# Performance work log

Hardware: AMD Instinct MI355X
Metric: run time of the kernel (lower is better)

The kernel has to match this reference:

```python
import jax, jax.numpy as jnp
import numpy as np

NUM_HEADS = 16

def setup_inputs() -> dict:
    key = jax.random.key(0)
    ks = jax.random.split(key, 8)
    B, S, D = 2, 2048, 1024
    w = lambda k: jax.random.normal(k, (D, D), dtype=jnp.float32) * 0.02
    return {
        "x": jax.random.normal(ks[0], (B, S, D), dtype=jnp.float32),
        "attn_mask": jnp.zeros((S, S), dtype=jnp.float32),
        "key_padding_mask": jnp.zeros((B, S), dtype=bool),
        "Wq": w(ks[1]), "bq": jnp.zeros((D,), jnp.float32),
        "Wk": w(ks[2]), "bk": jnp.zeros((D,), jnp.float32),
        "Wv": w(ks[3]), "bv": jnp.zeros((D,), jnp.float32),
        "Wg": w(ks[4]), "bg": jnp.full((D,), 0.5, jnp.float32),  # gate_bias_init=0.5
        "Wo": w(ks[5]), "bo": jnp.zeros((D,), jnp.float32),
    }

def reference(x, attn_mask, key_padding_mask, Wq, bq, Wk, bk, Wv, bv, Wg, bg, Wo, bo):
    B, S, D = x.shape
    H = NUM_HEADS
    hd = D // H
    scale = jnp.sqrt(jnp.float32(hd)).astype(x.dtype)

    def split_heads(t):  # (B,S,D) -> (B,H,S,hd)
        return t.reshape(B, S, H, hd).transpose(0, 2, 1, 3)

    q = split_heads(x @ Wq + bq)
    k = split_heads(x @ Wk + bk)
    v = split_heads(x @ Wv + bv)

    scores = jnp.einsum("bhqd,bhkd->bhqk", q, k) / scale
    scores = scores + attn_mask[None, None, :, :]
    scores = jnp.where(key_padding_mask[:, None, None, :], -jnp.inf, scores)

    attn_weights = jax.nn.softmax(scores, axis=-1)          # (B,H,S,S)
    attn_out = jnp.einsum("bhqk,bhkd->bhqd", attn_weights, v)

    gate = jax.nn.sigmoid(x @ Wg + bg)                      # (B,S,D)
    gate = split_heads(gate)                                # (B,H,S,hd)
    attn_out = attn_out * gate

    attn_out = attn_out.transpose(0, 2, 1, 3).reshape(B, S, D)
    output = attn_out @ Wo + bo
    avg_attn = attn_weights.mean(axis=1)                    # (B,S,S)
    return output, avg_attn
```

## Files before the change

kernel.cpp:

```cpp
#include <hip/hip_runtime.h>
#include <hip/hip_bf16.h>

#define LOG2E 1.4426950408889634f

typedef short short8 __attribute__((ext_vector_type(8)));
typedef float floatx4 __attribute__((ext_vector_type(4)));

__device__ __forceinline__ floatx4 mfma16(short8 a, short8 b, floatx4 c) {
    return __builtin_amdgcn_mfma_f32_16x16x32_bf16(a, b, c, 0, 0, 0);
}

__device__ __forceinline__ float fexp2(float x) { return __builtin_amdgcn_exp2f(x); }

__device__ __forceinline__ short f2bf(float f) {
    unsigned u = __builtin_bit_cast(unsigned, f);
    u += 0x7FFFu + ((u >> 16) & 1u);
    return (short)(u >> 16);
}
__device__ __forceinline__ unsigned bfpair(float a, float b) {
    unsigned ua = __builtin_bit_cast(unsigned, a);
    unsigned ub = __builtin_bit_cast(unsigned, b);
    ua += 0x7FFFu + ((ua >> 16) & 1u);
    ub += 0x7FFFu + ((ub >> 16) & 1u);
    return (ua >> 16) | (ub & 0xFFFF0000u);
}
__device__ __forceinline__ float bf2f(short s) {
    unsigned u = ((unsigned)(unsigned short)s) << 16;
    return __builtin_bit_cast(float, u);
}

__device__ __forceinline__ void glds16(const void* g, void* l) {
    __builtin_amdgcn_global_load_lds(
        (const __attribute__((address_space(1))) void*)g,
        (__attribute__((address_space(3))) void*)l, 16, 0, 0);
}

__device__ __forceinline__ short8 cvt8(const float* __restrict__ p) {
    float4 a = *reinterpret_cast<const float4*>(p);
    float4 b = *reinterpret_cast<const float4*>(p + 4);
    short8 r;
    r[0] = f2bf(a.x); r[1] = f2bf(a.y); r[2] = f2bf(a.z); r[3] = f2bf(a.w);
    r[4] = f2bf(b.x); r[5] = f2bf(b.y); r[6] = f2bf(b.z); r[7] = f2bf(b.w);
    return r;
}

__global__ __launch_bounds__(256) void cvt_x_kernel(
    const float* __restrict__ in, short* __restrict__ out, int n8)
{
    int i = blockIdx.x * blockDim.x + threadIdx.x;
    if (i < n8)
        *reinterpret_cast<short8*>(out + (size_t)i * 8) = cvt8(in + (size_t)i * 8);
}

__global__ __launch_bounds__(256) void cvt_wt_kernel(
    const float* __restrict__ W0, const float* __restrict__ W1,
    const float* __restrict__ W2, const float* __restrict__ W3,
    const float* __restrict__ W4, short* __restrict__ Wt)
{
    __shared__ short T[64 * 66];
    const int w = blockIdx.z;
    const float* W = (w == 0) ? W0 : (w == 1) ? W1 : (w == 2) ? W2 : (w == 3) ? W3 : W4;
    short* dst = Wt + (size_t)w * 1024 * 1024;
    const int kb = blockIdx.y * 64, nb = blockIdx.x * 64;
    const int t = threadIdx.x;
    const int r = t >> 2, c4 = (t & 3) * 16;
    *reinterpret_cast<short8*>(T + r * 66 + c4)     = cvt8(W + (size_t)(kb + r) * 1024 + nb + c4);
    *reinterpret_cast<short8*>(T + r * 66 + c4 + 8) = cvt8(W + (size_t)(kb + r) * 1024 + nb + c4 + 8);
    __syncthreads();
    short8 o0, o1;
    #pragma unroll
    for (int j = 0; j < 8; ++j) o0[j] = T[(c4 + j) * 66 + r];
    #pragma unroll
    for (int j = 0; j < 8; ++j) o1[j] = T[(c4 + 8 + j) * 66 + r];
    *reinterpret_cast<short8*>(dst + (size_t)(nb + r) * 1024 + kb + c4)     = o0;
    *reinterpret_cast<short8*>(dst + (size_t)(nb + r) * 1024 + kb + c4 + 8) = o1;
}

__global__ __launch_bounds__(256) void mask_prep(
    const float* __restrict__ amask, const unsigned char* __restrict__ kpm,
    float* __restrict__ Mc, int* __restrict__ flag)
{
    const int b = blockIdx.z, q = blockIdx.y;
    const int p0 = threadIdx.x * 8;
    float o[8];
    bool nz = false;
    #pragma unroll
    for (int i = 0; i < 8; ++i) {
        int p = p0 + i;
        int j = (p & ~31) | ((p >> 1) & 15) | ((p & 1) << 4);
        unsigned char kb = kpm[b * 2048 + j];
        float a = amask[(size_t)q * 2048 + j];
        nz |= (a != 0.f) || (kb != 0);
        o[i] = a * LOG2E + (kb ? -1.0e30f : 0.f);
    }
    float* dst = Mc + ((size_t)b * 2048 + q) * 2048 + p0;
    *reinterpret_cast<float4*>(dst)     = make_float4(o[0], o[1], o[2], o[3]);
    *reinterpret_cast<float4*>(dst + 4) = make_float4(o[4], o[5], o[6], o[7]);
    if (__ballot(nz) && ((threadIdx.x & 63) == 0)) atomicOr(flag, 1);
}

__device__ __forceinline__ void gemm_core(
    const short* __restrict__ A, const short* __restrict__ Wt,
    int mbase, int nbase, short* Asm, short* Bsm, floatx4 (&acc)[4][4])
{
    const int tid = threadIdx.x;
    const int lane = tid & 63, wid = tid >> 6;
    const int L15 = lane & 15, g = lane >> 4;
    const int wm = (wid >> 1) * 64, wn = (wid & 1) * 64;

    const int rowoff = lane >> 3;
    const int choff = ((lane & 7) ^ rowoff) * 8;
    const short* aP = A  + (size_t)(mbase + wid * 32 + rowoff) * 1024 + choff;
    const short* bP = Wt + (size_t)(nbase + wid * 32 + rowoff) * 1024 + choff;
    short* aL = Asm + wid * 2048;
    short* bL = Bsm + wid * 2048;

    const int xb = L15 & 7;
    const int s0 = (g ^ xb) * 8;
    const int s1 = ((g ^ 4) ^ xb) * 8;

    for (int kb = 0; kb < 1024; kb += 64) {
        __syncthreads();
        #pragma unroll
        for (int j = 0; j < 4; ++j) glds16(aP + kb + j * 8192, aL + j * 512);
        #pragma unroll
        for (int j = 0; j < 4; ++j) glds16(bP + kb + j * 8192, bL + j * 512);
        __syncthreads();
        #pragma unroll
        for (int ks = 0; ks < 2; ++ks) {
            const int so = ks ? s1 : s0;
            short8 af[4], bf[4];
            #pragma unroll
            for (int mt = 0; mt < 4; ++mt)
                af[mt] = *reinterpret_cast<const short8*>(Asm + (wm + mt * 16 + L15) * 64 + so);
            #pragma unroll
            for (int nt = 0; nt < 4; ++nt)
                bf[nt] = *reinterpret_cast<const short8*>(Bsm + (wn + nt * 16 + L15) * 64 + so);
            #pragma unroll
            for (int mt = 0; mt < 4; ++mt)
                #pragma unroll
                for (int nt = 0; nt < 4; ++nt)
                    acc[mt][nt] = mfma16(af[mt], bf[nt], acc[mt][nt]);
        }
    }
}

__global__ __launch_bounds__(256) void qkvg_gemm(
    const short* __restrict__ A, const short* __restrict__ Wt5,
    const float* __restrict__ b0, const float* __restrict__ b1,
    const float* __restrict__ b2, const float* __restrict__ b3,
    short* __restrict__ dQ, short* __restrict__ dK,
    short* __restrict__ dV, short* __restrict__ dG)
{
    __shared__ short Asm[128 * 64];
    __shared__ short Bsm[128 * 64];
    const int z = blockIdx.z;
    const int mbase = blockIdx.y * 128, nbase = blockIdx.x * 128;
    floatx4 acc[4][4] = {};
    gemm_core(A, Wt5 + (size_t)z * 1048576, mbase, nbase, Asm, Bsm, acc);

    const int lane = threadIdx.x & 63, wid = threadIdx.x >> 6;
    const int L15 = lane & 15, g = lane >> 4;
    const int wm = (wid >> 1) * 64, wn = (wid & 1) * 64;
    const float* bz = (z == 0) ? b0 : (z == 1) ? b1 : (z == 2) ? b2 : b3;
    short* dst = (z == 0) ? dQ : (z == 1) ? dK : (z == 2) ? dV : dG;

    #pragma unroll
    for (int nt = 0; nt < 4; ++nt) {
        int col = nbase + wn + nt * 16 + L15;
        float bv = bz[col];
        #pragma unroll
        for (int mt = 0; mt < 4; ++mt) {
            #pragma unroll
            for (int r = 0; r < 4; ++r) {
                int row = mbase + wm + mt * 16 + g * 4 + r;
                float val = acc[mt][nt][r] + bv;
                int bb = row >> 11, s = row & 2047;
                int hh = col >> 6, dh = col & 63;
                if (z <= 1) {
                    dst[(((size_t)bb * 16 + hh) * 2048 + s) * 64 + dh] = f2bf(val);
                } else if (z == 2) {
                    int sp = (s & ~31) | ((s & 15) << 1) | ((s >> 4) & 1);
                    dst[(((size_t)bb * 16 + hh) * 64 + dh) * 2048 + sp] = f2bf(val);
                } else {
                    float e = fexp2(-val * LOG2E);
                    dst[(size_t)row * 1024 + col] = f2bf(__builtin_amdgcn_rcpf(1.0f + e));
                }
            }
        }
    }
}

__global__ __launch_bounds__(256) void out_gemm(
    const short* __restrict__ A, const short* __restrict__ Wt,
    const float* __restrict__ bias, float* __restrict__ out)
{
    __shared__ short Asm[128 * 64];
    __shared__ short Bsm[128 * 64];
    const int mbase = blockIdx.y * 128, nbase = blockIdx.x * 128;
    floatx4 acc[4][4] = {};
    gemm_core(A, Wt, mbase, nbase, Asm, Bsm, acc);

    const int lane = threadIdx.x & 63, wid = threadIdx.x >> 6;
    const int L15 = lane & 15, g = lane >> 4;
    const int wm = (wid >> 1) * 64, wn = (wid & 1) * 64;
    #pragma unroll
    for (int nt = 0; nt < 4; ++nt) {
        int col = nbase + wn + nt * 16 + L15;
        float bv = bias[col];
        #pragma unroll
        for (int mt = 0; mt < 4; ++mt)
            #pragma unroll
            for (int r = 0; r < 4; ++r) {
                int row = mbase + wm + mt * 16 + g * 4 + r;
                out[(size_t)row * 1024 + col] = acc[mt][nt][r] + bv;
            }
    }
}

template<bool MASKED>
__device__ __forceinline__ void flash_body(
    const short* __restrict__ Q, const short* __restrict__ K,
    const short* __restrict__ Vt, const short* __restrict__ G,
    const float* __restrict__ Mc, short* __restrict__ att,
    float* __restrict__ inv_l,
    short* Ksm, short* Vsm, short* Psm)
{
    const int tid = threadIdx.x;
    const int lane = tid & 63, wid = tid >> 6;
    const int L15 = lane & 15, g = lane >> 4;
    const int b = blockIdx.z, h = blockIdx.x;
    const int bh = b * 16 + h;
    const int qb = blockIdx.y * 128 + wid * 16;
    const float SC = 0.125f * LOG2E;

    short8 aq0 = *reinterpret_cast<const short8*>(Q + ((size_t)bh * 2048 + qb + L15) * 64 + g * 8);
    short8 aq1 = *reinterpret_cast<const short8*>(Q + ((size_t)bh * 2048 + qb + L15) * 64 + 32 + g * 8);

    floatx4 O[4] = {};
    float l_r[4] = {0.f, 0.f, 0.f, 0.f};

    const int krow = lane >> 3;
    const int kch  = ((lane & 7) ^ krow) * 8;
    const bool isK = wid < 4;
    const int sw = isK ? wid : (wid - 4);
    const short* gP;
    if (isK) {
        gP = K + ((size_t)bh * 2048 + sw * 16 + krow) * 64 + kch;
    } else {
        const int vsc = (lane & 7) ^ krow;
        const int vhd = sw * 16 + 2 * krow + (vsc >> 2);
        gP = Vt + ((size_t)bh * 64 + vhd) * 2048 + (vsc & 3) * 8;
    }

    const int x7 = L15 & 7;
    const int sk0 = (g ^ x7) * 8, sk1 = ((g ^ 4) ^ x7) * 8;
    const int sv = (((L15 & 1) * 4 + g) ^ ((L15 >> 1) & 7)) * 8;
    const int vp = (L15 >> 1) * 64;

    short* Pw = Psm + wid * 1152;

    const float* mcP[4];
    float2 mc0[4], mc1[4];
    if (MASKED) {
        #pragma unroll
        for (int r = 0; r < 4; ++r) {
            mcP[r] = Mc + ((size_t)b * 2048 + qb + g * 4 + r) * 2048 + 2 * L15;
            mc0[r] = *reinterpret_cast<const float2*>(mcP[r]);
            mc1[r] = *reinterpret_cast<const float2*>(mcP[r] + 32);
        }
    }

    if (isK) {
        glds16(gP,       Ksm + sw * 1024);
        glds16(gP + 512, Ksm + sw * 1024 + 512);
    } else {
        glds16(gP,      Vsm + sw * 512);
        glds16(gP + 32, Vsm + 2048 + sw * 512);
    }

    for (int kb = 0; kb < 2048; kb += 64) {
        const int cur = (kb >> 6) & 1;
        __syncthreads();
        const int nb = kb + 64;
        const bool more = nb < 2048;
        float2 nmc0[4], nmc1[4];
        if (more) {
            if (isK) {
                glds16(gP + (size_t)nb * 64,       Ksm + (cur ^ 1) * 4096 + sw * 1024);
                glds16(gP + (size_t)nb * 64 + 512, Ksm + (cur ^ 1) * 4096 + sw * 1024 + 512);
            } else {
                glds16(gP + nb,      Vsm + (cur ^ 1) * 4096 + sw * 512);
                glds16(gP + nb + 32, Vsm + (cur ^ 1) * 4096 + 2048 + sw * 512);
            }
            if (MASKED) {
                #pragma unroll
                for (int r = 0; r < 4; ++r) {
                    nmc0[r] = *reinterpret_cast<const float2*>(mcP[r] + nb);
                    nmc1[r] = *reinterpret_cast<const float2*>(mcP[r] + nb + 32);
                }
            }
        }

        const short* Kb = Ksm + cur * 4096;
        floatx4 s[4];
        #pragma unroll
        for (int kt = 0; kt < 4; ++kt) {
            s[kt] = {};
            s[kt] = mfma16(aq0, *reinterpret_cast<const short8*>(Kb + (kt * 16 + L15) * 64 + sk0), s[kt]);
            s[kt] = mfma16(aq1, *reinterpret_cast<const short8*>(Kb + (kt * 16 + L15) * 64 + sk1), s[kt]);
        }

        #pragma unroll
        for (int r = 0; r < 4; ++r) {
            float e0 = fexp2(s[0][r] * SC + (MASKED ? mc0[r].x : 0.f));
            float e1 = fexp2(s[1][r] * SC + (MASKED ? mc0[r].y : 0.f));
            float e2 = fexp2(s[2][r] * SC + (MASKED ? mc1[r].x : 0.f));
            float e3 = fexp2(s[3][r] * SC + (MASKED ? mc1[r].y : 0.f));
            l_r[r] += (e0 + e1) + (e2 + e3);
            *reinterpret_cast<unsigned*>(&Pw[(g * 4 + r) * 72 + 2 * L15])      = bfpair(e0, e1);
            *reinterpret_cast<unsigned*>(&Pw[(g * 4 + r) * 72 + 32 + 2 * L15]) = bfpair(e2, e3);
        }
        short8 ap0 = *reinterpret_cast<const short8*>(&Pw[L15 * 72 + g * 8]);
        short8 ap1 = *reinterpret_cast<const short8*>(&Pw[L15 * 72 + 32 + g * 8]);
        const short* Vb0 = Vsm + cur * 4096;
        const short* Vb1 = Vb0 + 2048;
        #pragma unroll
        for (int t = 0; t < 4; ++t) {
            O[t] = mfma16(ap0, *reinterpret_cast<const short8*>(Vb0 + t * 512 + vp + sv), O[t]);
            O[t] = mfma16(ap1, *reinterpret_cast<const short8*>(Vb1 + t * 512 + vp + sv), O[t]);
        }

        if (MASKED && more) {
            #pragma unroll
            for (int r = 0; r < 4; ++r) { mc0[r] = nmc0[r]; mc1[r] = nmc1[r]; }
        }
    }

    float inv[4];
    #pragma unroll
    for (int r = 0; r < 4; ++r) {
        float ls = l_r[r];
        ls += __shfl_xor(ls, 1);
        ls += __shfl_xor(ls, 2);
        ls += __shfl_xor(ls, 4);
        ls += __shfl_xor(ls, 8);
        inv[r] = 1.0f / ls;
        if (L15 == 0) inv_l[(size_t)bh * 2048 + qb + g * 4 + r] = inv[r];
    }
    #pragma unroll
    for (int t = 0; t < 4; ++t) {
        int col = h * 64 + t * 16 + L15;
        #pragma unroll
        for (int r = 0; r < 4; ++r) {
            size_t qr = qb + g * 4 + r;
            float gt = bf2f(G[((size_t)b * 2048 + qr) * 1024 + col]);
            att[((size_t)b * 2048 + qr) * 1024 + col] = f2bf(O[t][r] * inv[r] * gt);
        }
    }
}

__global__ __launch_bounds__(512, 4) void flash_attn(
    const short* __restrict__ Q, const short* __restrict__ K,
    const short* __restrict__ Vt, const short* __restrict__ G,
    const float* __restrict__ Mc, const int* __restrict__ flag,
    short* __restrict__ att, float* __restrict__ inv_l)
{
    __shared__ short Ksm[2 * 4096];
    __shared__ short Vsm[2 * 4096];
    __shared__ short Psm[8 * 1152];
    if (*flag)
        flash_body<true>(Q, K, Vt, G, Mc, att, inv_l, Ksm, Vsm, Psm);
    else
        flash_body<false>(Q, K, Vt, G, Mc, att, inv_l, Ksm, Vsm, Psm);
}

__global__ __launch_bounds__(256) void avg_attn_kernel(
    const short* __restrict__ Q, const short* __restrict__ K,
    const float* __restrict__ inv_l, float* mca, const int* __restrict__ flag)
{
    __shared__ short Ksm[2][128 * 64];
    const int tid = threadIdx.x;
    const int lane = tid & 63, wid = tid >> 6;
    const int L15 = lane & 15, g = lane >> 4;
    const int b = blockIdx.z;
    const int qb = blockIdx.y * 64 + wid * 16;
    const int ks = blockIdx.x * 128;
    const float SC = 0.125f * LOG2E;

    float pm[4][2][4];
    if (*flag) {
        #pragma unroll
        for (int c = 0; c < 4; ++c)
            #pragma unroll
            for (int r = 0; r < 4; ++r) {
                size_t qr = qb + g * 4 + r;
                float2 m = *reinterpret_cast<const float2*>(
                    mca + ((size_t)b * 2048 + qr) * 2048 + ks + c * 32 + 2 * L15);
                pm[c][0][r] = m.x;
                pm[c][1][r] = m.y;
            }
    } else {
        #pragma unroll
        for (int c = 0; c < 4; ++c)
            #pragma unroll
            for (int r = 0; r < 4; ++r) {
                pm[c][0][r] = 0.f;
                pm[c][1][r] = 0.f;
            }
    }
    float av[4][2][4] = {};

    const int rowoff = lane >> 3;
    const int choff = ((lane & 7) ^ rowoff) * 8;
    const int x7 = L15 & 7;
    const int sk0 = (g ^ x7) * 8, sk1 = ((g ^ 4) ^ x7) * 8;
    short* kL[2] = { &Ksm[0][wid * 2048], &Ksm[1][wid * 2048] };

    {
        const short* p = K + ((size_t)(b * 16) * 2048 + ks + wid * 32 + rowoff) * 64 + choff;
        #pragma unroll
        for (int j = 0; j < 4; ++j) glds16(p + j * 512, kL[0] + j * 512);
    }
    short8 aq0 = *reinterpret_cast<const short8*>(Q + ((size_t)(b * 16) * 2048 + qb + L15) * 64 + g * 8);
    short8 aq1 = *reinterpret_cast<const short8*>(Q + ((size_t)(b * 16) * 2048 + qb + L15) * 64 + 32 + g * 8);
    float iv[4];
    #pragma unroll
    for (int r = 0; r < 4; ++r) iv[r] = inv_l[(size_t)(b * 16) * 2048 + qb + g * 4 + r];

    for (int h = 0; h < 16; ++h) {
        __syncthreads();
        short8 naq0, naq1;
        float niv[4];
        if (h < 15) {
            int nbh = b * 16 + h + 1;
            const short* p = K + ((size_t)nbh * 2048 + ks + wid * 32 + rowoff) * 64 + choff;
            #pragma unroll
            for (int j = 0; j < 4; ++j) glds16(p + j * 512, kL[(h + 1) & 1] + j * 512);
            naq0 = *reinterpret_cast<const short8*>(Q + ((size_t)nbh * 2048 + qb + L15) * 64 + g * 8);
            naq1 = *reinterpret_cast<const short8*>(Q + ((size_t)nbh * 2048 + qb + L15) * 64 + 32 + g * 8);
            #pragma unroll
            for (int r = 0; r < 4; ++r) niv[r] = inv_l[(size_t)nbh * 2048 + qb + g * 4 + r];
        }

        const short* Kb = Ksm[h & 1];
        #pragma unroll
        for (int c = 0; c < 4; ++c) {
            const short* kbase = Kb + c * 32 * 64;
            floatx4 s0 = {}, s1 = {};
            s0 = mfma16(aq0, *reinterpret_cast<const short8*>(kbase + L15 * 64 + sk0), s0);
            s0 = mfma16(aq1, *reinterpret_cast<const short8*>(kbase + L15 * 64 + sk1), s0);
            s1 = mfma16(aq0, *reinterpret_cast<const short8*>(kbase + (16 + L15) * 64 + sk0), s1);
            s1 = mfma16(aq1, *reinterpret_cast<const short8*>(kbase + (16 + L15) * 64 + sk1), s1);
            #pragma unroll
            for (int r = 0; r < 4; ++r) {
                av[c][0][r] += fexp2(s0[r] * SC + pm[c][0][r]) * iv[r];
                av[c][1][r] += fexp2(s1[r] * SC + pm[c][1][r]) * iv[r];
            }
        }
        if (h < 15) {
            aq0 = naq0; aq1 = naq1;
            #pragma unroll
            for (int r = 0; r < 4; ++r) iv[r] = niv[r];
        }
    }
    #pragma unroll
    for (int c = 0; c < 4; ++c)
        #pragma unroll
        for (int t = 0; t < 2; ++t)
            #pragma unroll
            for (int r = 0; r < 4; ++r) {
                size_t qr = qb + g * 4 + r;
                int col = ks + c * 32 + t * 16 + L15;
                mca[((size_t)b * 2048 + qr) * 2048 + col] = av[c][t][r] * 0.0625f;
            }
}

extern "C" void kernel_launch(void* const* d_in, const int* in_sizes, int n_in,
                              void* d_out, int out_size, void* d_ws, size_t ws_size,
                              hipStream_t stream)
{
    const float* x  = (const float*)d_in[0];
    const float* amask = (const float*)d_in[1];
    const unsigned char* kpm = (const unsigned char*)d_in[2];
    const float* Wq = (const float*)d_in[3];
    const float* bq = (const float*)d_in[4];
    const float* Wk = (const float*)d_in[5];
    const float* bk = (const float*)d_in[6];
    const float* Wv = (const float*)d_in[7];
    const float* bv = (const float*)d_in[8];
    const float* Wg = (const float*)d_in[9];
    const float* bg = (const float*)d_in[10];
    const float* Wo = (const float*)d_in[11];
    const float* bo = (const float*)d_in[12];

    char* ws = (char*)d_ws;
    const size_t MB = 1u << 20;
    short* Xb    = (short*)(ws);
    short* Att   = Xb;
    short* Qw    = (short*)(ws + 8 * MB);
    short* Kw    = (short*)(ws + 16 * MB);
    short* Vt    = (short*)(ws + 24 * MB);
    short* Gw    = (short*)(ws + 32 * MB);
    short* Wt    = (short*)(ws + 40 * MB);
    float* stats = (float*)(ws + 50 * MB);
    int*   flagp = (int*)(ws + 50 * MB + 262144);

    float* outp = (float*)d_out;
    float* avgp = (float*)d_out + 4194304;

    hipMemsetAsync(flagp, 0, sizeof(int), stream);

    cvt_x_kernel<<<2048, 256, 0, stream>>>(x, Xb, 524288);
    cvt_wt_kernel<<<dim3(16, 16, 5), 256, 0, stream>>>(Wq, Wk, Wv, Wg, Wo, Wt);
    mask_prep<<<dim3(1, 2048, 2), 256, 0, stream>>>(amask, kpm, avgp, flagp);

    qkvg_gemm<<<dim3(8, 32, 4), 256, 0, stream>>>(Xb, Wt, bq, bk, bv, bg, Qw, Kw, Vt, Gw);

    flash_attn<<<dim3(16, 16, 2), 512, 0, stream>>>(Qw, Kw, Vt, Gw, avgp, flagp, Att, stats);

    avg_attn_kernel<<<dim3(16, 32, 2), 256, 0, stream>>>(Qw, Kw, stats, avgp, flagp);

    out_gemm<<<dim3(8, 32), 256, 0, stream>>>(Att, Wt + 4 * 1048576, bo, outp);
}
```

Before: 296.0 us.

## Use 256x256 double-buffered tiles with XCD-aware block swizzle in QKVG GEMM

Reworks the fused QKV/gate projection GEMM so that 512-thread blocks compute 256x256 output tiles. LDS is double-buffered so the next K-slice loads while the current one is multiplied. Blocks are mapped to tiles with a modulo-8 swizzle, likely to keep related tiles on the same XCD for L2 reuse. Separately, s_setprio is raised around the MFMA sections in the GEMM, flash attention and avg-attn kernels to favour matrix-issue waves. The larger tiles cut global traffic per FLOP, but they use more registers and LDS per block and launch only 256 blocks, which lowers occupancy and risks load imbalance.

```diff
diff --git a/kernel.cpp b/kernel.cpp
--- a/kernel.cpp
+++ b/kernel.cpp
@@ -99,6 +99,65 @@
     if (__ballot(nz) && ((threadIdx.x & 63) == 0)) atomicOr(flag, 1);
 }
 
+__device__ __forceinline__ void gemm_core256(
+    const short* __restrict__ A, const short* __restrict__ Wt,
+    int mbase, int nbase, short* Asm, short* Bsm, floatx4 (&acc)[8][4])
+{
+    const int tid = threadIdx.x;
+    const int lane = tid & 63, wid = tid >> 6;
+    const int L15 = lane & 15, g = lane >> 4;
+    const int wrow = (wid >> 2) * 128, wcol = (wid & 3) * 64;
+
+    const int rl = lane >> 3;
+    const int ch = ((lane & 7) ^ rl) * 8;
+    const short* aP = A  + (size_t)(mbase + wid * 32 + rl) * 1024 + ch;
+    const short* bP = Wt + (size_t)(nbase + wid * 32 + rl) * 1024 + ch;
+
+    const int xb = L15 & 7;
+    const int s0 = (g ^ xb) * 8;
+    const int s1 = ((g ^ 4) ^ xb) * 8;
+
+    #pragma unroll
+    for (int j = 0; j < 4; ++j) glds16(aP + j * 8192, Asm + wid * 2048 + j * 512);
+    #pragma unroll
+    for (int j = 0; j < 4; ++j) glds16(bP + j * 8192, Bsm + wid * 2048 + j * 512);
+    __syncthreads();
+
+    for (int t = 0; t < 16; ++t) {
+        const int cur = t & 1;
+        const short* Ab = Asm + cur * 16384;
+        const short* Bb = Bsm + cur * 16384;
+        if (t < 15) {
+            const int kb = (t + 1) * 64;
+            short* aL = Asm + (cur ^ 1) * 16384 + wid * 2048;
+            short* bL = Bsm + (cur ^ 1) * 16384 + wid * 2048;
+            #pragma unroll
+            for (int j = 0; j < 4; ++j) glds16(aP + kb + j * 8192, aL + j * 512);
+            #pragma unroll
+            for (int j = 0; j < 4; ++j) glds16(bP + kb + j * 8192, bL + j * 512);
+        }
+        #pragma unroll
+        for (int ks = 0; ks < 2; ++ks) {
+            const int so = ks ? s1 : s0;
+            short8 af[8], bf[4];
+            #pragma unroll
+            for (int mt = 0; mt < 8; ++mt)
+                af[mt] = *reinterpret_cast<const short8*>(Ab + (wrow + mt * 16 + L15) * 64 + so);
+            #pragma unroll
+            for (int nt = 0; nt < 4; ++nt)
+                bf[nt] = *reinterpret_cast<const short8*>(Bb + (wcol + nt * 16 + L15) * 64 + so);
+            __builtin_amdgcn_s_setprio(1);
+            #pragma unroll
+            for (int mt = 0; mt < 8; ++mt)
+                #pragma unroll
+                for (int nt = 0; nt < 4; ++nt)
+                    acc[mt][nt] = mfma16(af[mt], bf[nt], acc[mt][nt]);
+            __builtin_amdgcn_s_setprio(0);
+        }
+        __syncthreads();
+    }
+}
+
 __device__ __forceinline__ void gemm_core(
     const short* __restrict__ A, const short* __restrict__ Wt,
     int mbase, int nbase, short* Asm, short* Bsm, floatx4 (&acc)[4][4])
@@ -145,35 +204,40 @@
     }
 }
 
-__global__ __launch_bounds__(256) void qkvg_gemm(
+__global__ __launch_bounds__(512) void qkvg_gemm(
     const short* __restrict__ A, const short* __restrict__ Wt5,
     const float* __restrict__ b0, const float* __restrict__ b1,
     const float* __restrict__ b2, const float* __restrict__ b3,
     short* __restrict__ dQ, short* __restrict__ dK,
     short* __restrict__ dV, short* __restrict__ dG)
 {
-    __shared__ short Asm[128 * 64];
-    __shared__ short Bsm[128 * 64];
-    const int z = blockIdx.z;
-    const int mbase = blockIdx.y * 128, nbase = blockIdx.x * 128;
-    floatx4 acc[4][4] = {};
-    gemm_core(A, Wt5 + (size_t)z * 1048576, mbase, nbase, Asm, Bsm, acc);
+    __shared__ short Asm[2 * 16384];
+    __shared__ short Bsm[2 * 16384];
+
+    const int wg = blockIdx.x;
+    const int swz = (wg & 7) * 32 + (wg >> 3);
+    const int z = swz >> 6;
+    const int rem = swz & 63;
+    const int mbase = (rem >> 2) * 256, nbase = (rem & 3) * 256;
+
+    floatx4 acc[8][4] = {};
+    gemm_core256(A, Wt5 + (size_t)z * 1048576, mbase, nbase, Asm, Bsm, acc);
 
     const int lane = threadIdx.x & 63, wid = threadIdx.x >> 6;
     const int L15 = lane & 15, g = lane >> 4;
-    const int wm = (wid >> 1) * 64, wn = (wid & 1) * 64;
+    const int wrow = (wid >> 2) * 128, wcol = (wid & 3) * 64;
     const float* bz = (z == 0) ? b0 : (z == 1) ? b1 : (z == 2) ? b2 : b3;
     short* dst = (z == 0) ? dQ : (z == 1) ? dK : (z == 2) ? dV : dG;
 
     #pragma unroll
     for (int nt = 0; nt < 4; ++nt) {
-        int col = nbase + wn + nt * 16 + L15;
+        int col = nbase + wcol + nt * 16 + L15;
         float bv = bz[col];
         #pragma unroll
-        for (int mt = 0; mt < 4; ++mt) {
+        for (int mt = 0; mt < 8; ++mt) {
             #pragma unroll
             for (int r = 0; r < 4; ++r) {
-                int row = mbase + wm + mt * 16 + g * 4 + r;
+                int row = mbase + wrow + mt * 16 + g * 4 + r;
                 float val = acc[mt][nt][r] + bv;
                 int bb = row >> 11, s = row & 2047;
                 int hh = col >> 6, dh = col & 63;
@@ -304,12 +368,14 @@
 
         const short* Kb = Ksm + cur * 4096;
         floatx4 s[4];
+        __builtin_amdgcn_s_setprio(1);
         #pragma unroll
         for (int kt = 0; kt < 4; ++kt) {
             s[kt] = {};
             s[kt] = mfma16(aq0, *reinterpret_cast<const short8*>(Kb + (kt * 16 + L15) * 64 + sk0), s[kt]);
             s[kt] = mfma16(aq1, *reinterpret_cast<const short8*>(Kb + (kt * 16 + L15) * 64 + sk1), s[kt]);
         }
+        __builtin_amdgcn_s_setprio(0);
 
         #pragma unroll
         for (int r = 0; r < 4; ++r) {
@@ -325,11 +391,13 @@
         short8 ap1 = *reinterpret_cast<const short8*>(&Pw[L15 * 72 + 32 + g * 8]);
         const short* Vb0 = Vsm + cur * 4096;
         const short* Vb1 = Vb0 + 2048;
+        __builtin_amdgcn_s_setprio(1);
         #pragma unroll
         for (int t = 0; t < 4; ++t) {
             O[t] = mfma16(ap0, *reinterpret_cast<const short8*>(Vb0 + t * 512 + vp + sv), O[t]);
             O[t] = mfma16(ap1, *reinterpret_cast<const short8*>(Vb1 + t * 512 + vp + sv), O[t]);
         }
+        __builtin_amdgcn_s_setprio(0);
 
         if (MASKED && more) {
             #pragma unroll
@@ -448,10 +516,12 @@
         for (int c = 0; c < 4; ++c) {
             const short* kbase = Kb + c * 32 * 64;
             floatx4 s0 = {}, s1 = {};
+            __builtin_amdgcn_s_setprio(1);
             s0 = mfma16(aq0, *reinterpret_cast<const short8*>(kbase + L15 * 64 + sk0), s0);
             s0 = mfma16(aq1, *reinterpret_cast<const short8*>(kbase + L15 * 64 + sk1), s0);
             s1 = mfma16(aq0, *reinterpret_cast<const short8*>(kbase + (16 + L15) * 64 + sk0), s1);
             s1 = mfma16(aq1, *reinterpret_cast<const short8*>(kbase + (16 + L15) * 64 + sk1), s1);
+            __builtin_amdgcn_s_setprio(0);
             #pragma unroll
             for (int r = 0; r < 4; ++r) {
                 av[c][0][r] += fexp2(s0[r] * SC + pm[c][0][r]) * iv[r];
@@ -515,7 +585,7 @@
     cvt_wt_kernel<<<dim3(16, 16, 5), 256, 0, stream>>>(Wq, Wk, Wv, Wg, Wo, Wt);
     mask_prep<<<dim3(1, 2048, 2), 256, 0, stream>>>(amask, kpm, avgp, flagp);
 
-    qkvg_gemm<<<dim3(8, 32, 4), 256, 0, stream>>>(Xb, Wt, bq, bk, bv, bg, Qw, Kw, Vt, Gw);
+    qkvg_gemm<<<256, 512, 0, stream>>>(Xb, Wt, bq, bk, bv, bg, Qw, Kw, Vt, Gw);
 
     flash_attn<<<dim3(16, 16, 2), 512, 0, stream>>>(Qw, Kw, Vt, Gw, avgp, flagp, Att, stats);
 
```

Result: slower. 303.3 us (+2.5%).

## Rewrite QKVG GEMM with 256x256 tiles and 4-stage async LDS pipeline

Applied to the files above, without the earlier changes.

Replaces the QKVG projection GEMM core with a 256x256 tile per 512-thread block. It stages A/B through a 4-deep ring of shared-memory buffers using direct global-to-LDS loads, with explicit vmcnt waits and barriers, and raises priority around the MFMA bursts. Blocks are launched as a 1D grid with an XCD-style swizzle, and the epilogue is split per output kind so the loop order suits each layout. This aims to hide global-load latency and improve data reuse. The cost is much larger LDS use (128 KB) and more accumulator registers, which can limit occupancy. It also relies on the existing glds16 helper.

```diff
diff --git a/kernel.cpp b/kernel.cpp
--- a/kernel.cpp
+++ b/kernel.cpp
@@ -99,6 +99,72 @@
     if (__ballot(nz) && ((threadIdx.x & 63) == 0)) atomicOr(flag, 1);
 }
 
+__device__ __forceinline__ void gemm_core256p(
+    const short* __restrict__ A, const short* __restrict__ Wt,
+    int mbase, int nbase, short* Asm, short* Bsm, floatx4 (&acc)[8][4])
+{
+    const int tid = threadIdx.x;
+    const int lane = tid & 63, wid = tid >> 6;
+    const int L15 = lane & 15, g = lane >> 4;
+    const int wrow = (wid >> 2) * 128, wcol = (wid & 3) * 64;
+
+    const int rl4 = lane >> 2, c4 = lane & 3;
+    const int R0 = wid * 32;
+    const short* aG = A  + (size_t)(mbase + R0 + rl4) * 1024 + c4 * 8;
+    const short* bG = Wt + (size_t)(nbase + R0 + rl4) * 1024 + c4 * 8;
+
+#define STAGE(t_) do {                                                        \
+        const int sl_ = (t_) & 3;                                             \
+        glds16(aG + (size_t)(t_) * 32,         Asm + sl_ * 8192 + R0 * 32);   \
+        glds16(aG + (size_t)(t_) * 32 + 16384, Asm + sl_ * 8192 + R0 * 32 + 512); \
+        glds16(bG + (size_t)(t_) * 32,         Bsm + sl_ * 8192 + R0 * 32);   \
+        glds16(bG + (size_t)(t_) * 32 + 16384, Bsm + sl_ * 8192 + R0 * 32 + 512); \
+    } while (0)
+
+#define COMP(t_) do {                                                         \
+        const int sl_ = (t_) & 3;                                             \
+        const short* Ab_ = Asm + sl_ * 8192;                                  \
+        const short* Bb_ = Bsm + sl_ * 8192;                                  \
+        short8 af_[8], bf_[4];                                                \
+        _Pragma("unroll")                                                     \
+        for (int mt = 0; mt < 8; ++mt)                                        \
+            af_[mt] = *reinterpret_cast<const short8*>(Ab_ + (wrow + mt * 16 + L15) * 32 + g * 8); \
+        _Pragma("unroll")                                                     \
+        for (int nt = 0; nt < 4; ++nt)                                        \
+            bf_[nt] = *reinterpret_cast<const short8*>(Bb_ + (wcol + nt * 16 + L15) * 32 + g * 8); \
+        __builtin_amdgcn_s_setprio(1);                                        \
+        _Pragma("unroll")                                                     \
+        for (int mt = 0; mt < 8; ++mt)                                        \
+            _Pragma("unroll")                                                 \
+            for (int nt = 0; nt < 4; ++nt)                                    \
+                acc[mt][nt] = mfma16(af_[mt], bf_[nt], acc[mt][nt]);          \
+        __builtin_amdgcn_s_setprio(0);                                        \
+    } while (0)
+
+#define BARRIER_SB() do {                                                     \
+        __builtin_amdgcn_sched_barrier(0);                                    \
+        __builtin_amdgcn_s_barrier();                                         \
+        __builtin_amdgcn_sched_barrier(0);                                    \
+    } while (0)
+
+    STAGE(0); STAGE(1); STAGE(2);
+
+    for (int t = 0; t < 29; ++t) {
+        BARRIER_SB();
+        STAGE(t + 3);
+        asm volatile("s_waitcnt vmcnt(12)" ::: "memory");
+        BARRIER_SB();
+        COMP(t);
+    }
+    BARRIER_SB(); asm volatile("s_waitcnt vmcnt(8)" ::: "memory"); BARRIER_SB(); COMP(29);
+    BARRIER_SB(); asm volatile("s_waitcnt vmcnt(4)" ::: "memory"); BARRIER_SB(); COMP(30);
+    BARRIER_SB(); asm volatile("s_waitcnt vmcnt(0)" ::: "memory"); BARRIER_SB(); COMP(31);
+
+#undef STAGE
+#undef COMP
+#undef BARRIER_SB
+}
+
 __device__ __forceinline__ void gemm_core(
     const short* __restrict__ A, const short* __restrict__ Wt,
     int mbase, int nbase, short* Asm, short* Bsm, floatx4 (&acc)[4][4])
@@ -145,45 +211,78 @@
     }
 }
 
-__global__ __launch_bounds__(256) void qkvg_gemm(
+__global__ __launch_bounds__(512) void qkvg_gemm(
     const short* __restrict__ A, const short* __restrict__ Wt5,
     const float* __restrict__ b0, const float* __restrict__ b1,
     const float* __restrict__ b2, const float* __restrict__ b3,
     short* __restrict__ dQ, short* __restrict__ dK,
     short* __restrict__ dV, short* __restrict__ dG)
 {
-    __shared__ short Asm[128 * 64];
-    __shared__ short Bsm[128 * 64];
-    const int z = blockIdx.z;
-    const int mbase = blockIdx.y * 128, nbase = blockIdx.x * 128;
-    floatx4 acc[4][4] = {};
-    gemm_core(A, Wt5 + (size_t)z * 1048576, mbase, nbase, Asm, Bsm, acc);
+    __shared__ short Asm[4 * 8192];
+    __shared__ short Bsm[4 * 8192];
+
+    const int wg = blockIdx.x;
+    const int swz = (wg & 7) * 32 + (wg >> 3);
+    const int z = swz >> 6;
+    const int rem = swz & 63;
+    const int mbase = (rem >> 2) * 256, nbase = (rem & 3) * 256;
+
+    floatx4 acc[8][4] = {};
+    gemm_core256p(A, Wt5 + (size_t)z * 1048576, mbase, nbase, Asm, Bsm, acc);
 
     const int lane = threadIdx.x & 63, wid = threadIdx.x >> 6;
     const int L15 = lane & 15, g = lane >> 4;
-    const int wm = (wid >> 1) * 64, wn = (wid & 1) * 64;
+    const int wrow = (wid >> 2) * 128, wcol = (wid & 3) * 64;
     const float* bz = (z == 0) ? b0 : (z == 1) ? b1 : (z == 2) ? b2 : b3;
     short* dst = (z == 0) ? dQ : (z == 1) ? dK : (z == 2) ? dV : dG;
 
-    #pragma unroll
-    for (int nt = 0; nt < 4; ++nt) {
-        int col = nbase + wn + nt * 16 + L15;
-        float bv = bz[col];
-        #pragma unroll
-        for (int mt = 0; mt < 4; ++mt) {
+    float bvv[4];
+    #pragma unroll
+    for (int nt = 0; nt < 4; ++nt) bvv[nt] = bz[nbase + wcol + nt * 16 + L15];
+
+    if (z <= 1) {
+        #pragma unroll
+        for (int mt = 0; mt < 8; ++mt) {
             #pragma unroll
             for (int r = 0; r < 4; ++r) {
-                int row = mbase + wm + mt * 16 + g * 4 + r;
-                float val = acc[mt][nt][r] + bv;
+                int row = mbase + wrow + mt * 16 + g * 4 + r;
                 int bb = row >> 11, s = row & 2047;
-                int hh = col >> 6, dh = col & 63;
-                if (z <= 1) {
-                    dst[(((size_t)bb * 16 + hh) * 2048 + s) * 64 + dh] = f2bf(val);
-                } else if (z == 2) {
+                #pragma unroll
+                for (int nt = 0; nt < 4; ++nt) {
+                    int col = nbase + wcol + nt * 16 + L15;
+                    int hh = col >> 6, dh = col & 63;
+                    dst[(((size_t)bb * 16 + hh) * 2048 + s) * 64 + dh] =
+                        f2bf(acc[mt][nt][r] + bvv[nt]);
+                }
+            }
+        }
+    } else if (z == 2) {
+        #pragma unroll
+        for (int nt = 0; nt < 4; ++nt) {
+            int col = nbase + wcol + nt * 16 + L15;
+            int hh = col >> 6, dh = col & 63;
+            #pragma unroll
+            for (int mt = 0; mt < 8; ++mt) {
+                #pragma unroll
+                for (int r = 0; r < 4; ++r) {
+                    int row = mbase + wrow + mt * 16 + g * 4 + r;
+                    int bb = row >> 11, s = row & 2047;
                     int sp = (s & ~31) | ((s & 15) << 1) | ((s >> 4) & 1);
-                    dst[(((size_t)bb * 16 + hh) * 64 + dh) * 2048 + sp] = f2bf(val);
-                } else {
-                    float e = fexp2(-val * LOG2E);
+                    dst[(((size_t)bb * 16 + hh) * 64 + dh) * 2048 + sp] =
+                        f2bf(acc[mt][nt][r] + bvv[nt]);
+                }
+            }
+        }
+    } else {
+        #pragma unroll
+        for (int mt = 0; mt < 8; ++mt) {
+            #pragma unroll
+            for (int r = 0; r < 4; ++r) {
+                int row = mbase + wrow + mt * 16 + g * 4 + r;
+                #pragma unroll
+                for (int nt = 0; nt < 4; ++nt) {
+                    int col = nbase + wcol + nt * 16 + L15;
+                    float e = fexp2(-(acc[mt][nt][r] + bvv[nt]) * LOG2E);
                     dst[(size_t)row * 1024 + col] = f2bf(__builtin_amdgcn_rcpf(1.0f + e));
                 }
             }
@@ -515,7 +614,7 @@
     cvt_wt_kernel<<<dim3(16, 16, 5), 256, 0, stream>>>(Wq, Wk, Wv, Wg, Wo, Wt);
     mask_prep<<<dim3(1, 2048, 2), 256, 0, stream>>>(amask, kpm, avgp, flagp);
 
-    qkvg_gemm<<<dim3(8, 32, 4), 256, 0, stream>>>(Xb, Wt, bq, bk, bv, bg, Qw, Kw, Vt, Gw);
+    qkvg_gemm<<<256, 512, 0, stream>>>(Xb, Wt, bq, bk, bv, bg, Qw, Kw, Vt, Gw);
 
     flash_attn<<<dim3(16, 16, 2), 512, 0, stream>>>(Qw, Kw, Vt, Gw, avgp, flagp, Att, stats);
 
```

Result: faster. 286.3 us (-3.3%).
